# Kernel tuning notes

Hardware: AMD Instinct MI355X
Metric: run time of the kernel (lower is better)

Reference implementation:

```python
import jax, jax.numpy as jnp
import numpy as np

N = 50000          # residues
E = 1000000        # edges
H = 128            # hidden_channels
CUT = 11.5         # cutoff
NR = 6             # num_radial
NS = 3             # num_spherical
NPE = 16           # num_pos_emb

def swish(x):
    return x * jax.nn.sigmoid(x)

def rbf(d):
    # Bessel-style radial basis with smooth cosine cutoff, [E, NR]
    u = jnp.clip(d / CUT, 0.0, 1.0)
    n = jnp.arange(1, NR + 1, dtype=jnp.float32)
    fc = 0.5 * (jnp.cos(jnp.pi * u) + 1.0)
    return jnp.sqrt(2.0 / CUT) * jnp.sin(n * jnp.pi * u[:, None]) / (d[:, None] + 1e-6) * fc[:, None]

def angle_emb(d, ang):
    # d_angle_emb: radial x cos(l*angle) -> [E, NR*NS]
    r = rbf(d)
    l = jnp.arange(NS, dtype=jnp.float32)
    a = jnp.cos(ang[:, None] * l)
    return (r[:, :, None] * a[:, None, :]).reshape(d.shape[0], NR * NS)

def theta_phi_emb(d, theta, phi):
    # d_theta_phi_emb: radial x angular(theta) x angular(phi) -> [E, NR*NS*NS]
    r = rbf(d)
    l = jnp.arange(NS, dtype=jnp.float32)
    ct = jnp.cos(theta[:, None] * l)
    cp = jnp.cos(phi[:, None] * l)
    return jnp.einsum('en,el,em->enlm', r, ct, cp).reshape(d.shape[0], NR * NS * NS)


def setup_inputs():
    key = jax.random.key(0)
    ks = jax.random.split(key, 20)
    f32 = jnp.float32
    pos = jax.random.normal(ks[0], (N, 3), f32) * 8.0
    pos_n = pos + jax.random.normal(ks[1], (N, 3), f32) * 0.8
    pos_c = pos + jax.random.normal(ks[2], (N, 3), f32) * 0.8
    z = jax.random.randint(ks[3], (N,), 0, 26)
    bb_embs = jax.random.normal(ks[4], (N, 6), f32)
    side_chain_embs = jax.random.normal(ks[5], (N, 8), f32)
    esm_embs = jax.random.normal(ks[6], (N, 1280), f32)
    batch = jnp.zeros((N,), jnp.int32)
    edge_index = jax.random.randint(ks[7], (2, E), 0, N)
    def w(k, shape):
        return jax.random.normal(k, shape, f32) * (1.0 / np.sqrt(shape[0]))
    edge_in = NR * NS * NS + 3 * NR * NS + NPE  # 54 + 54 + 16 = 124
    params = dict(
        W_emb=w(ks[8], (26 + 6 + 8, H // 2)), b_emb=jnp.zeros((H // 2,), f32),
        W_esm=w(ks[9], (1280, H // 2)), b_esm=jnp.zeros((H // 2,), f32),
        W_edge=w(ks[10], (edge_in, H)),
        W_msg=w(ks[11], (H, H)),
        W_upd=w(ks[12], (H, H)),
        W_o0=w(ks[13], (H, H)), b_o0=jnp.zeros((H,), f32),
        W_o1=w(ks[14], (H, 32)), b_o1=jnp.zeros((32,), f32),
        W_of=w(ks[15], (32, 1)), b_of=jnp.zeros((1,), f32),
        W_n0=w(ks[16], (H, 32)), b_n0=jnp.zeros((32,), f32),
        W_nf=w(ks[17], (32, 2)), b_nf=jnp.zeros((2,), f32),
    )
    return dict(z=z, pos=pos, pos_n=pos_n, pos_c=pos_c, bb_embs=bb_embs,
                side_chain_embs=side_chain_embs, esm_embs=esm_embs,
                batch=batch, edge_index=edge_index, **params)


def reference(z, pos, pos_n, pos_c, bb_embs, side_chain_embs, esm_embs, batch,
              edge_index, W_emb, b_emb, W_esm, b_esm, W_edge, W_msg, W_upd,
              W_o0, b_o0, W_o1, b_o1, W_of, b_of, W_n0, b_n0, W_nf, b_nf):
    # --- node embedding fusion (level='allatom+esm') ---
    oh = jax.nn.one_hot(z, 26, dtype=jnp.float32)
    x_a = jnp.concatenate([oh, bb_embs, side_chain_embs], axis=1) @ W_emb + b_emb
    x_s = esm_embs @ W_esm + b_esm
    x = jnp.concatenate([x_a, x_s], axis=-1)  # [N, H]

    j, i = edge_index[0], edge_index[1]

    # --- sinusoidal positional embedding of sequence offsets ---
    dpe = (j - i).astype(jnp.float32)
    freq = jnp.exp(jnp.arange(0, NPE, 2, dtype=jnp.float32) * (-np.log(10000.0) / NPE))
    ang = dpe[:, None] * freq
    pe = jnp.concatenate([jnp.cos(ang), jnp.sin(ang)], axis=-1)  # [E, NPE]

    # --- distance / theta / phi (triplet gathers via sequence neighbors) ---
    v_ji = pos[j] - pos[i]
    dist = jnp.linalg.norm(pos[i] - pos[j], axis=1)
    refi0 = (i - 1) % N
    refi1 = (i + 1) % N
    v_r0 = pos[refi0] - pos[i]
    v_r1 = pos[refi1] - pos[i]
    a = jnp.sum(v_ji * v_r0, axis=-1)
    b = jnp.linalg.norm(jnp.cross(v_ji, v_r0), axis=-1)
    theta = jnp.arctan2(b, a)
    p1 = jnp.cross(v_r0, v_r1)
    p2 = jnp.cross(v_r0, v_ji)
    a = jnp.sum(p1 * p2, axis=-1)
    b = jnp.sum(jnp.cross(p1, p2) * v_r0, axis=-1) / (jnp.linalg.norm(v_r0, axis=-1) + 1e-7)
    phi = jnp.arctan2(b, a)
    feature0 = theta_phi_emb(dist, theta, phi)  # [E, 54]

    # --- backbone-frame Euler angles (allatom branch) ---
    o1x = pos_n[i] - pos[i]
    o1z = jnp.cross(o1x, jnp.cross(o1x, pos_c[i] - pos[i]))
    o1zl = jnp.linalg.norm(o1z, axis=1) + 1e-7
    o2x = pos_n[j] - pos[j]
    o2z = jnp.cross(o2x, jnp.cross(o2x, pos_c[j] - pos[j]))
    o2zl = jnp.linalg.norm(o2z, axis=1) + 1e-7
    nvec = jnp.cross(o1z, o2z)
    angle1 = jnp.arctan2(jnp.sum(jnp.cross(o1x, nvec) * o1z, -1) / o1zl, jnp.sum(o1x * nvec, -1))
    angle2 = jnp.arctan2(jnp.linalg.norm(nvec, axis=-1), jnp.sum(o1z * o2z, -1))
    angle3 = jnp.arctan2(jnp.sum(jnp.cross(nvec, o2x) * o2z, -1) / o2zl, jnp.sum(nvec * o2x, -1))
    feature1 = jnp.concatenate([angle_emb(dist, angle1), angle_emb(dist, angle2),
                                angle_emb(dist, angle3)], axis=1)  # [E, 54]

    # --- message passing (gather-compute-scatter stand-in for model_E) ---
    ef = swish(jnp.concatenate([feature0, feature1, pe], axis=-1) @ W_edge)  # [E, H]
    m = swish(x[j] @ W_msg) * ef
    agg = jax.ops.segment_sum(m, i, num_segments=N)
    xe = x + swish(agg @ W_upd)

    # --- output heads (dropout inactive at inference) ---
    xn = jax.nn.relu(x @ W_n0 + b_n0)
    node_out = xn @ W_nf + b_nf                   # [N, 2]
    h = jax.nn.relu(xe @ W_o0 + b_o0)
    h = jax.nn.relu(h @ W_o1 + b_o1)
    out = jax.nn.sigmoid(h @ W_of + b_of)         # [N, 1]
    return out, node_out
```

## Files before the change

kernel.cpp:

```cpp
#include <hip/hip_runtime.h>
#include <math.h>
#include <stdint.h>

#define NRES 50000
#define NEDGE 1000000
#define PI_F 3.14159265358979323846f
#define NSEG 196

typedef __attribute__((ext_vector_type(8))) short short8;
typedef __attribute__((ext_vector_type(4))) float floatx4;
typedef __attribute__((ext_vector_type(2))) short bf16x2;
typedef __attribute__((address_space(1))) bf16x2* gbf16x2p;

struct f3 { float x, y, z; };
__device__ __forceinline__ f3 ld3(const float* __restrict__ p, int i) {
  return {p[3*i+0], p[3*i+1], p[3*i+2]};
}
__device__ __forceinline__ f3 f3sub(f3 a, f3 b){ return {a.x-b.x, a.y-b.y, a.z-b.z}; }
__device__ __forceinline__ f3 f3cross(f3 a, f3 b){
  return {a.y*b.z - a.z*b.y, a.z*b.x - a.x*b.z, a.x*b.y - a.y*b.x};
}
__device__ __forceinline__ float f3dot(f3 a, f3 b){ return a.x*b.x + a.y*b.y + a.z*b.z; }
__device__ __forceinline__ float swish_fast(float v){
  return v * __builtin_amdgcn_rcpf(1.0f + __expf(-v));
}
__device__ __forceinline__ short f2bf(float f){
  unsigned u = __float_as_uint(f);
  unsigned r = (u + 0x7fffu + ((u >> 16) & 1u)) >> 16;
  return (short)r;
}
__device__ __forceinline__ float bf2f(short s){
  return __uint_as_float(((unsigned)(unsigned short)s) << 16);
}
__device__ __forceinline__ float cos_atan2(float y, float x){
  return x * __builtin_amdgcn_rsqf(fmaxf(x*x + y*y, 1e-30f));
}
__device__ __forceinline__ void atom_pk_bf16(short* addr, bf16x2 v){
  __builtin_amdgcn_global_atomic_fadd_v2bf16((gbf16x2p)(uintptr_t)addr, v);
}
__device__ __forceinline__ unsigned pkbf(float lo, float hi){
  unsigned r;
  asm("v_cvt_pk_bf16_f32 %0, %1, %2" : "=v"(r) : "v"(lo), "v"(hi));
  return r;
}

struct EdgeGeo {
  float rb[6];
  float ct, cp, ca1, ca2, ca3;
  float dpe;
};
__device__ __forceinline__ EdgeGeo edge_geo(
    int j, int i,
    const float* __restrict__ pos, const float* __restrict__ posn,
    const float* __restrict__ posc)
{
  EdgeGeo g;
  f3 pj = ld3(pos, j), pi = ld3(pos, i);
  f3 vji = f3sub(pj, pi);
  float nji2 = f3dot(vji, vji);
  float dist = sqrtf(nji2);
  int r0i = (i == 0) ? (NRES - 1) : (i - 1);
  int r1i = (i == NRES - 1) ? 0 : (i + 1);
  f3 vr0 = f3sub(ld3(pos, r0i), pi);
  f3 vr1 = f3sub(ld3(pos, r1i), pi);
  float nr02 = f3dot(vr0, vr0);

  g.ct = f3dot(vji, vr0) * __builtin_amdgcn_rsqf(fmaxf(nji2 * nr02, 1e-30f));
  f3 p1 = f3cross(vr0, vr1);
  f3 p2 = f3cross(vr0, vji);
  float pa = f3dot(p1, p2);
  float pb = f3dot(f3cross(p1, p2), vr0) / (sqrtf(nr02) + 1e-7f);
  g.cp = cos_atan2(pb, pa);

  f3 pni = ld3(posn, i), pci = ld3(posc, i);
  f3 o1x = f3sub(pni, pi);
  f3 o1z = f3cross(o1x, f3cross(o1x, f3sub(pci, pi)));
  float no1z2 = f3dot(o1z, o1z);
  float o1zl = sqrtf(no1z2) + 1e-7f;
  f3 pnj = ld3(posn, j), pcj = ld3(posc, j);
  f3 o2x = f3sub(pnj, pj);
  f3 o2z = f3cross(o2x, f3cross(o2x, f3sub(pcj, pj)));
  float no2z2 = f3dot(o2z, o2z);
  float o2zl = sqrtf(no2z2) + 1e-7f;
  f3 nv = f3cross(o1z, o2z);
  float y1 = f3dot(f3cross(o1x, nv), o1z) / o1zl;
  g.ca1 = cos_atan2(y1, f3dot(o1x, nv));
  g.ca2 = f3dot(o1z, o2z) * __builtin_amdgcn_rsqf(fmaxf(no1z2 * no2z2, 1e-30f));
  float y3 = f3dot(f3cross(nv, o2x), o2z) / o2zl;
  g.ca3 = cos_atan2(y3, f3dot(nv, o2x));

  float u = fminf(dist * (1.0f/11.5f), 1.0f);
  float spu, cpu;
  __sincosf(PI_F * u, &spu, &cpu);
  float fc = 0.5f * (cpu + 1.0f);
  float pref = 0.41702882811414954f * __builtin_amdgcn_rcpf(dist + 1e-6f) * fc;
  {
    float twoc = 2.0f * cpu;
    float s_nm1 = 0.0f, s_n = spu;
    #pragma unroll
    for (int nn = 0; nn < 6; ++nn) {
      g.rb[nn] = pref * s_n;
      float s_np1 = twoc * s_n - s_nm1;
      s_nm1 = s_n; s_n = s_np1;
    }
  }
  g.dpe = (float)(j - i);
  return g;
}

__device__ __forceinline__ float feat_val(const EdgeGeo& g, int f,
                                          const float* ctv, const float* cpv,
                                          const float* cav1, const float* cav2,
                                          const float* cav3)
{
  if (f < 54) {
    int nn = f / 9, l = (f % 9) / 3, m = f % 3;
    return g.rb[nn] * ctv[l] * cpv[m];
  } else {
    int ff = f - 54;
    int t = ff / 18, nn = (ff % 18) / 3, l = ff % 3;
    const float* cav = (t == 0) ? cav1 : (t == 1) ? cav2 : cav3;
    return g.rb[nn] * cav[l];
  }
}

__device__ __forceinline__ void edge_features_full(
    int e, int j, int i,
    const float* __restrict__ pos, const float* __restrict__ posn,
    const float* __restrict__ posc, short (*sF)[136])
{
  EdgeGeo g = edge_geo(j, i, pos, posn, posc);
  float ctv[3]  = {1.0f, g.ct,  2.0f*g.ct*g.ct  - 1.0f};
  float cpv[3]  = {1.0f, g.cp,  2.0f*g.cp*g.cp  - 1.0f};
  float cav1[3] = {1.0f, g.ca1, 2.0f*g.ca1*g.ca1 - 1.0f};
  float cav2[3] = {1.0f, g.ca2, 2.0f*g.ca2*g.ca2 - 1.0f};
  float cav3[3] = {1.0f, g.ca3, 2.0f*g.ca3*g.ca3 - 1.0f};
  #pragma unroll
  for (int f = 0; f < 108; f += 2) {
    float v0 = feat_val(g, f,     ctv, cpv, cav1, cav2, cav3);
    float v1 = feat_val(g, f + 1, ctv, cpv, cav1, cav2, cav3);
    *(unsigned*)&sF[e][f] = pkbf(v0, v1);
  }
  const float FRQ[8] = {1.0f, 0.31622776601683794f, 0.1f, 0.03162277660168379f,
                        0.01f, 0.003162277660168379f, 0.001f, 0.0003162277660168379f};
  float cb[8], sb[8];
  #pragma unroll
  for (int q = 0; q < 8; ++q) __sincosf(g.dpe * FRQ[q], &sb[q], &cb[q]);
  #pragma unroll
  for (int q = 0; q < 8; q += 2) {
    *(unsigned*)&sF[e][108 + q] = pkbf(cb[q], cb[q+1]);
    *(unsigned*)&sF[e][116 + q] = pkbf(sb[q], sb[q+1]);
  }
  *(unsigned*)&sF[e][124] = 0u;
  *(unsigned*)&sF[e][126] = 0u;
}

__device__ __forceinline__ void edge_features_q(
    int e, int j, int i, int q,
    const float* __restrict__ pos, const float* __restrict__ posn,
    const float* __restrict__ posc, short (*sF)[136])
{
  EdgeGeo g = edge_geo(j, i, pos, posn, posc);
  float ctv[3]  = {1.0f, g.ct,  2.0f*g.ct*g.ct  - 1.0f};
  float cpv[3]  = {1.0f, g.cp,  2.0f*g.cp*g.cp  - 1.0f};
  float cav1[3] = {1.0f, g.ca1, 2.0f*g.ca1*g.ca1 - 1.0f};
  float cav2[3] = {1.0f, g.ca2, 2.0f*g.ca2*g.ca2 - 1.0f};
  float cav3[3] = {1.0f, g.ca3, 2.0f*g.ca3*g.ca3 - 1.0f};

  if (q == 0) {
    #pragma unroll
    for (int f = 0; f < 28; f += 2)
      *(unsigned*)&sF[e][f] = pkbf(feat_val(g, f, ctv, cpv, cav1, cav2, cav3),
                                   feat_val(g, f+1, ctv, cpv, cav1, cav2, cav3));
  } else if (q == 1) {
    #pragma unroll
    for (int f = 28; f < 54; f += 2)
      *(unsigned*)&sF[e][f] = pkbf(feat_val(g, f, ctv, cpv, cav1, cav2, cav3),
                                   feat_val(g, f+1, ctv, cpv, cav1, cav2, cav3));
    const float FRQ[8] = {1.0f, 0.31622776601683794f, 0.1f, 0.03162277660168379f,
                          0.01f, 0.003162277660168379f, 0.001f, 0.0003162277660168379f};
    float cb[8], sb[8];
    #pragma unroll
    for (int p = 0; p < 8; ++p) __sincosf(g.dpe * FRQ[p], &sb[p], &cb[p]);
    #pragma unroll
    for (int p = 0; p < 8; p += 2) {
      *(unsigned*)&sF[e][108 + p] = pkbf(cb[p], cb[p+1]);
      *(unsigned*)&sF[e][116 + p] = pkbf(sb[p], sb[p+1]);
    }
    *(unsigned*)&sF[e][124] = 0u;
    *(unsigned*)&sF[e][126] = 0u;
  } else if (q == 2) {
    #pragma unroll
    for (int f = 54; f < 80; f += 2)
      *(unsigned*)&sF[e][f] = pkbf(feat_val(g, f, ctv, cpv, cav1, cav2, cav3),
                                   feat_val(g, f+1, ctv, cpv, cav1, cav2, cav3));
  } else {
    #pragma unroll
    for (int f = 80; f < 108; f += 2)
      *(unsigned*)&sF[e][f] = pkbf(feat_val(g, f, ctv, cpv, cav1, cav2, cav3),
                                   feat_val(g, f+1, ctv, cpv, cav1, cav2, cav3));
  }
}

__global__ __launch_bounds__(256) void k_wprep(
    const float* __restrict__ We, const float* __restrict__ Wm,
    const float* __restrict__ Ws, const float* __restrict__ Wu,
    const float* __restrict__ Wo0, const float* __restrict__ Wn0,
    const float* __restrict__ Wo1,
    short* __restrict__ Wef, short* __restrict__ Wmf, short* __restrict__ Wsf,
    short* __restrict__ Wuf, short* __restrict__ Wo0f,
    short* __restrict__ Wn0f, short* __restrict__ Wo1f)
{
  int gid = blockIdx.x * 256 + threadIdx.x;
  const float* src; short* dst; int NT, K, N, t;
  if      (gid < 16384)  { t = gid;          src = We;  dst = Wef;  NT = 8; K = 124;  N = 128; }
  else if (gid < 32768)  { t = gid - 16384;  src = Wm;  dst = Wmf;  NT = 8; K = 128;  N = 128; }
  else if (gid < 114688) { t = gid - 32768;  src = Ws;  dst = Wsf;  NT = 4; K = 1280; N = 64;  }
  else if (gid < 131072) { t = gid - 114688; src = Wu;  dst = Wuf;  NT = 8; K = 128;  N = 128; }
  else if (gid < 147456) { t = gid - 131072; src = Wo0; dst = Wo0f; NT = 8; K = 128;  N = 128; }
  else if (gid < 151552) { t = gid - 147456; src = Wn0; dst = Wn0f; NT = 2; K = 128;  N = 32;  }
  else if (gid < 155648) { t = gid - 151552; src = Wo1; dst = Wo1f; NT = 2; K = 128;  N = 32;  }
  else return;
  int j = t & 7, lane = (t >> 3) & 63;
  int rest = t >> 9;
  int nt = rest % NT, kt = rest / NT;
  int k = kt*32 + (lane >> 4)*8 + j, n = nt*16 + (lane & 15);
  dst[t] = f2bf((k < K) ? src[k*N + n] : 0.0f);
}

__global__ __launch_bounds__(256) void k_hist(
    const int* __restrict__ ei, int* __restrict__ bins)
{
  int e = blockIdx.x * 256 + threadIdx.x;
  if (e < NEDGE) atomicAdd(&bins[ei[NEDGE + e]], 1);
}

__global__ __launch_bounds__(256) void k_scan1(
    int* __restrict__ bins, int* __restrict__ bsum)
{
  __shared__ int s[256];
  const int t = threadIdx.x, b = blockIdx.x;
  const int idx = b * 256 + t;
  int v = (idx < NRES) ? bins[idx] : 0;
  s[t] = v;
  __syncthreads();
  #pragma unroll
  for (int d = 1; d < 256; d <<= 1) {
    int add = (t >= d) ? s[t - d] : 0;
    __syncthreads();
    if (t >= d) s[t] += add;
    __syncthreads();
  }
  if (idx < NRES) bins[idx] = s[t] - v;
  if (t == 255) bsum[b] = s[255];
}

__global__ __launch_bounds__(256) void k_scan2(int* __restrict__ bsum)
{
  __shared__ int s[256];
  const int t = threadIdx.x;
  int v = (t < NSEG) ? bsum[t] : 0;
  s[t] = v;
  __syncthreads();
  #pragma unroll
  for (int d = 1; d < 256; d <<= 1) {
    int add = (t >= d) ? s[t - d] : 0;
    __syncthreads();
    if (t >= d) s[t] += add;
    __syncthreads();
  }
  if (t < NSEG) bsum[t] = s[t] - v;
}

__global__ __launch_bounds__(256) void k_scatter(
    const int* __restrict__ ei, int* __restrict__ bins,
    const int* __restrict__ bsum, int2* __restrict__ sij)
{
  int e = blockIdx.x * 256 + threadIdx.x;
  if (e < NEDGE) {
    int j = ei[e], i = ei[NEDGE + e];
    int slot = atomicAdd(&bins[i], 1) + bsum[i >> 8];
    if (slot >= 0 && slot < NEDGE) sij[slot] = make_int2(j, i);
  }
}

__global__ __launch_bounds__(256) void k_xa(
    const int* __restrict__ z, const float* __restrict__ bb,
    const float* __restrict__ side, const float* __restrict__ W_emb,
    const float* __restrict__ b_emb, short* __restrict__ xb)
{
  int tid = threadIdx.x;
  int h = tid & 63;
  int n = blockIdx.x * 4 + (tid >> 6);
  if (n >= NRES) return;
  int zz = z[n];
  float acc = W_emb[zz * 64 + h] + b_emb[h];
  #pragma unroll
  for (int k = 0; k < 6; ++k) acc += bb[n*6 + k] * W_emb[(26 + k)*64 + h];
  #pragma unroll
  for (int k = 0; k < 8; ++k) acc += side[n*8 + k] * W_emb[(32 + k)*64 + h];
  xb[(size_t)n * 128 + h] = f2bf(acc);
}

__global__ __launch_bounds__(256) void k_esm(
    const float* __restrict__ esm, const short* __restrict__ Wsf,
    const float* __restrict__ b, short* __restrict__ xb)
{
  const int tid = threadIdx.x;
  const int lane = tid & 63, w = tid >> 6;
  const int quad = lane >> 4, colb = lane & 15;
  const int tile0 = blockIdx.x * 64 + w * 16;

  int arow = tile0 + colb;
  if (arow >= NRES) arow = NRES - 1;
  const float* ap = esm + (size_t)arow * 1280 + quad * 8;

  floatx4 acc[4];
  #pragma unroll
  for (int nt = 0; nt < 4; ++nt) acc[nt] = (floatx4){0.f, 0.f, 0.f, 0.f};

  for (int kt = 0; kt < 40; ++kt) {
    float4 v0 = *(const float4*)(ap + kt*32);
    float4 v1 = *(const float4*)(ap + kt*32 + 4);
    short8 a;
    a[0] = f2bf(v0.x); a[1] = f2bf(v0.y); a[2] = f2bf(v0.z); a[3] = f2bf(v0.w);
    a[4] = f2bf(v1.x); a[5] = f2bf(v1.y); a[6] = f2bf(v1.z); a[7] = f2bf(v1.w);
    #pragma unroll
    for (int nt = 0; nt < 4; ++nt) {
      short8 bf = *(const short8*)&Wsf[(size_t)((kt*4 + nt)*64 + lane)*8];
      acc[nt] = __builtin_amdgcn_mfma_f32_16x16x32_bf16(a, bf, acc[nt], 0, 0, 0);
    }
  }
  #pragma unroll
  for (int nt = 0; nt < 4; ++nt) {
    int ch = nt*16 + colb;
    float bias = b[ch];
    #pragma unroll
    for (int r = 0; r < 4; ++r) {
      int n = tile0 + quad*4 + r;
      if (n < NRES) xb[(size_t)n * 128 + 64 + ch] = f2bf(acc[nt][r] + bias);
    }
  }
}

__global__ __launch_bounds__(512) void k_node(
    const float* __restrict__ esm, const short* __restrict__ Wsf,
    const float* __restrict__ b_esm,
    const int* __restrict__ z, const float* __restrict__ bb,
    const float* __restrict__ side, const float* __restrict__ W_emb,
    const float* __restrict__ b_emb,
    const short* __restrict__ Wmf,
    short* __restrict__ xb, short* __restrict__ xmb)
{
  __shared__ __align__(16) short sE[2][64][72];
  __shared__ __align__(16) short sX[64][136];

  const int tid = threadIdx.x;
  const int lane = tid & 63, w = tid >> 6;
  const int quad = lane >> 4, colb = lane & 15;
  const int n0 = blockIdx.x * 64;

  const int lrow = tid >> 3;
  const int p0 = tid & 7, p1 = p0 + 8;
  int grow = n0 + lrow; if (grow >= NRES) grow = NRES - 1;
  const float* rbase = esm + (size_t)grow * 1280;

  const int rt = w & 3;
  const int ct0 = (w >> 2) * 2, ct1 = ct0 + 1;

  floatx4 acc0 = (floatx4){0.f,0.f,0.f,0.f};
  floatx4 acc1 = (floatx4){0.f,0.f,0.f,0.f};

  {
    float4 va = *(const float4*)(rbase + p0*4);
    float4 vb = *(const float4*)(rbase + p1*4);
    *(unsigned*)&sE[0][lrow][p0*4]     = pkbf(va.x, va.y);
    *(unsigned*)&sE[0][lrow][p0*4 + 2] = pkbf(va.z, va.w);
    *(unsigned*)&sE[0][lrow][p1*4]     = pkbf(vb.x, vb.y);
    *(unsigned*)&sE[0][lrow][p1*4 + 2] = pkbf(vb.z, vb.w);
  }
  __syncthreads();

  for (int s = 0; s < 20; ++s) {
    float4 va = {0.f,0.f,0.f,0.f}, vb = {0.f,0.f,0.f,0.f};
    if (s < 19) {
      va = *(const float4*)(rbase + (s+1)*64 + p0*4);
      vb = *(const float4*)(rbase + (s+1)*64 + p1*4);
    }
    const int buf = s & 1;
    #pragma unroll
    for (int kk = 0; kk < 2; ++kk) {
      short8 af = *(const short8*)&sE[buf][rt*16 + colb][kk*32 + quad*8];
      const int kc = s*2 + kk;
      short8 bf0 = *(const short8*)&Wsf[(size_t)((kc*4 + ct0)*64 + lane)*8];
      short8 bf1 = *(const short8*)&Wsf[(size_t)((kc*4 + ct1)*64 + lane)*8];
      acc0 = __builtin_amdgcn_mfma_f32_16x16x32_bf16(af, bf0, acc0, 0, 0, 0);
      acc1 = __builtin_amdgcn_mfma_f32_16x16x32_bf16(af, bf1, acc1, 0, 0, 0);
    }
    __syncthreads();
    if (s < 19) {
      const int nb = (s + 1) & 1;
      *(unsigned*)&sE[nb][lrow][p0*4]     = pkbf(va.x, va.y);
      *(unsigned*)&sE[nb][lrow][p0*4 + 2] = pkbf(va.z, va.w);
      *(unsigned*)&sE[nb][lrow][p1*4]     = pkbf(vb.x, vb.y);
      *(unsigned*)&sE[nb][lrow][p1*4 + 2] = pkbf(vb.z, vb.w);
      __syncthreads();
    }
  }

  {
    float bias0 = b_esm[ct0*16 + colb];
    float bias1 = b_esm[ct1*16 + colb];
    #pragma unroll
    for (int r = 0; r < 4; ++r) {
      int row = rt*16 + quad*4 + r;
      sX[row][64 + ct0*16 + colb] = f2bf(acc0[r] + bias0);
      sX[row][64 + ct1*16 + colb] = f2bf(acc1[r] + bias1);
    }
  }
  {
    int r2 = tid >> 3;
    int n2 = n0 + r2; if (n2 >= NRES) n2 = NRES - 1;
    int c0 = (tid & 7) * 8;
    int zz = z[n2];
    float bbv[6], sdv[8];
    #pragma unroll
    for (int k = 0; k < 6; ++k) bbv[k] = bb[n2*6 + k];
    #pragma unroll
    for (int k = 0; k < 8; ++k) sdv[k] = side[n2*8 + k];
    #pragma unroll
    for (int c = 0; c < 8; c += 2) {
      float u0, u1;
      #pragma unroll
      for (int h = 0; h < 2; ++h) {
        int col = c0 + c + h;
        float a2 = W_emb[zz*64 + col] + b_emb[col];
        #pragma unroll
        for (int k = 0; k < 6; ++k) a2 += bbv[k] * W_emb[(26 + k)*64 + col];
        #pragma unroll
        for (int k = 0; k < 8; ++k) a2 += sdv[k] * W_emb[(32 + k)*64 + col];
        if (h) u1 = a2; else u0 = a2;
      }
      *(unsigned*)&sX[r2][c0 + c] = pkbf(u0, u1);
    }
  }
  __syncthreads();

  #pragma unroll
  for (int it = 0; it < 2; ++it) {
    int idx = it * 512 + tid;
    int row = idx >> 4, c8 = idx & 15;
    int n = n0 + row;
    if (n < NRES) *(short8*)&xb[(size_t)n * 128 + c8*8] = *(const short8*)&sX[row][c8*8];
  }

  floatx4 accM[4];
  #pragma unroll
  for (int mt = 0; mt < 4; ++mt) accM[mt] = (floatx4){0.f,0.f,0.f,0.f};
  #pragma unroll
  for (int kt = 0; kt < 4; ++kt) {
    short8 b0 = *(const short8*)&Wmf[(size_t)((kt*8 + w)*64 + lane)*8];
    #pragma unroll
    for (int mt = 0; mt < 4; ++mt) {
      short8 a = *(const short8*)&sX[mt*16 + colb][kt*32 + quad*8];
      accM[mt] = __builtin_amdgcn_mfma_f32_16x16x32_bf16(a, b0, accM[mt], 0, 0, 0);
    }
  }
  __syncthreads();

  #pragma unroll
  for (int mt = 0; mt < 4; ++mt)
    #pragma unroll
    for (int r = 0; r < 4; ++r)
      sX[mt*16 + quad*4 + r][w*16 + colb] = f2bf(swish_fast(accM[mt][r]));
  __syncthreads();
  #pragma unroll
  for (int it = 0; it < 2; ++it) {
    int idx = it * 512 + tid;
    int row = idx >> 4, c8 = idx & 15;
    int n = n0 + row;
    if (n < NRES) *(short8*)&xmb[(size_t)n * 128 + c8*8] = *(const short8*)&sX[row][c8*8];
  }
}

__global__ __launch_bounds__(256, 4) void k_edge_s(
    const int2* __restrict__ sij,
    const float* __restrict__ pos,
    const float* __restrict__ posn, const float* __restrict__ posc,
    const short* __restrict__ xmb, const short* __restrict__ Wef,
    short* __restrict__ aggb)
{
  __shared__ int sJ[64];
  __shared__ int sI[64];
  __shared__ __align__(16) short sF[64][136];
  __shared__ __align__(16) short sXJ[64][136];

  const int tid = threadIdx.x;
  const int orig = blockIdx.x;
  const int xcd = orig & 7, sub = orig >> 3;
  const int wg = (xcd == 0 ? 0 : 1954 + (xcd - 1) * 1953) + sub;
  const int e0 = wg * 64;

  if (tid < 64) {
    int2 ji = sij[e0 + tid];
    int jj = ji.x, ii = ji.y;
    sJ[tid] = (jj < 0) ? 0 : ((jj >= NRES) ? NRES - 1 : jj);
    sI[tid] = (ii < 0) ? 0 : ((ii >= NRES) ? NRES - 1 : ii);
  }
  __syncthreads();

  {
    const int e = tid & 63, q = tid >> 6;
    edge_features_q(e, sJ[e], sI[e], q, pos, posn, posc, sF);
  }
  #pragma unroll
  for (int it = 0; it < 4; ++it) {
    int idx = it * 256 + tid;
    int row = idx >> 4;
    int c8 = idx & 15;
    *(short8*)&sXJ[row][c8*8] = *(const short8*)&xmb[(size_t)sJ[row] * 128 + c8*8];
  }
  __syncthreads();

  const int lane = tid & 63, w = tid >> 6;
  const int quad = lane >> 4, colb = lane & 15;
  const int nb = w * 2;

  short8 bE[4][2];
  #pragma unroll
  for (int kt = 0; kt < 4; ++kt)
    #pragma unroll
    for (int nt = 0; nt < 2; ++nt)
      bE[kt][nt] = *(const short8*)&Wef[(size_t)((kt*8 + nb + nt)*64 + lane)*8];

  floatx4 accE[4][2];
  #pragma unroll
  for (int mt = 0; mt < 4; ++mt) {
    accE[mt][0] = (floatx4){0.f, 0.f, 0.f, 0.f};
    accE[mt][1] = (floatx4){0.f, 0.f, 0.f, 0.f};
  }

  #pragma unroll
  for (int kt = 0; kt < 4; ++kt) {
    #pragma unroll
    for (int mt = 0; mt < 4; ++mt) {
      short8 af = *(const short8*)&sF[mt*16 + colb][kt*32 + quad*8];
      #pragma unroll
      for (int nt = 0; nt < 2; ++nt)
        accE[mt][nt] = __builtin_amdgcn_mfma_f32_16x16x32_bf16(af, bE[kt][nt], accE[mt][nt], 0, 0, 0);
    }
  }
  __syncthreads();

  short (*sM)[136] = sF;
  #pragma unroll
  for (int mt = 0; mt < 4; ++mt)
    #pragma unroll
    for (int nt = 0; nt < 2; ++nt) {
      int ch = w*32 + nt*16 + colb;
      #pragma unroll
      for (int r = 0; r < 4; ++r) {
        int e = mt*16 + quad*4 + r;
        float mv = bf2f(sXJ[e][ch]) * swish_fast(accE[mt][nt][r]);
        sM[e][ch] = f2bf(mv);
      }
    }
  __syncthreads();

  {
    const int p = tid & 63;
    const int g = tid >> 6;
    float ax = 0.f, ay = 0.f;
    int cur = sI[g * 16];
    #pragma unroll
    for (int rr = 0; rr < 16; ++rr) {
      int row = g * 16 + rr;
      int ii = sI[row];
      if (ii != cur) {
        bf16x2 v; v[0] = f2bf(ax); v[1] = f2bf(ay);
        atom_pk_bf16(&aggb[(size_t)cur * 128 + p*2], v);
        ax = 0.f; ay = 0.f; cur = ii;
      }
      bf16x2 mv = *(const bf16x2*)&sM[row][p*2];
      ax += bf2f(mv[0]); ay += bf2f(mv[1]);
    }
    bf16x2 v; v[0] = f2bf(ax); v[1] = f2bf(ay);
    atom_pk_bf16(&aggb[(size_t)cur * 128 + p*2], v);
  }
}

__global__ __launch_bounds__(256, 4) void k_edge_b(
    const int* __restrict__ ei, const float* __restrict__ pos,
    const float* __restrict__ posn, const float* __restrict__ posc,
    const short* __restrict__ xb, const short* __restrict__ Wef,
    const short* __restrict__ Wmf, short* __restrict__ aggb)
{
  __shared__ int sJ[64];
  __shared__ int sI[64];
  __shared__ __align__(16) short sF[64][136];
  __shared__ __align__(16) short sXJ[64][136];

  const int tid = threadIdx.x;
  const int e0 = blockIdx.x * 64;

  if (tid < 64) { sJ[tid] = ei[e0 + tid]; sI[tid] = ei[NEDGE + e0 + tid]; }
  __syncthreads();

  if (tid < 64) {
    edge_features_full(tid, sJ[tid], sI[tid], pos, posn, posc, sF);
  } else {
    const int t2 = tid - 64;
    for (int it = 0; it < 6; ++it) {
      int idx = it * 192 + t2;
      if (idx < 1024) {
        int row = idx >> 4;
        int c8 = idx & 15;
        *(short8*)&sXJ[row][c8*8] = *(const short8*)&xb[(size_t)sJ[row] * 128 + c8*8];
      }
    }
  }
  __syncthreads();

  const int lane = tid & 63, w = tid >> 6;
  const int quad = lane >> 4, colb = lane & 15;
  const int nb = w * 2;

  short8 bE[4][2], bM[4][2];
  #pragma unroll
  for (int kt = 0; kt < 4; ++kt)
    #pragma unroll
    for (int nt = 0; nt < 2; ++nt) {
      bE[kt][nt] = *(const short8*)&Wef[(size_t)((kt*8 + nb + nt)*64 + lane)*8];
      bM[kt][nt] = *(const short8*)&Wmf[(size_t)((kt*8 + nb + nt)*64 + lane)*8];
    }

  floatx4 accE[4][2], accM[4][2];
  #pragma unroll
  for (int mt = 0; mt < 4; ++mt)
    #pragma unroll
    for (int nt = 0; nt < 2; ++nt) {
      accE[mt][nt] = (floatx4){0.f, 0.f, 0.f, 0.f};
      accM[mt][nt] = (floatx4){0.f, 0.f, 0.f, 0.f};
    }

  #pragma unroll
  for (int kt = 0; kt < 4; ++kt) {
    #pragma unroll
    for (int mt = 0; mt < 4; ++mt) {
      short8 af = *(const short8*)&sF [mt*16 + colb][kt*32 + quad*8];
      short8 ax = *(const short8*)&sXJ[mt*16 + colb][kt*32 + quad*8];
      #pragma unroll
      for (int nt = 0; nt < 2; ++nt) {
        accE[mt][nt] = __builtin_amdgcn_mfma_f32_16x16x32_bf16(af, bE[kt][nt], accE[mt][nt], 0, 0, 0);
        accM[mt][nt] = __builtin_amdgcn_mfma_f32_16x16x32_bf16(ax, bM[kt][nt], accM[mt][nt], 0, 0, 0);
      }
    }
  }
  __syncthreads();

  short (*sM)[136] = sXJ;
  #pragma unroll
  for (int mt = 0; mt < 4; ++mt)
    #pragma unroll
    for (int nt = 0; nt < 2; ++nt) {
      int ch = w*32 + nt*16 + colb;
      #pragma unroll
      for (int r = 0; r < 4; ++r) {
        int e = mt*16 + quad*4 + r;
        sM[e][ch] = f2bf(swish_fast(accM[mt][nt][r]) * swish_fast(accE[mt][nt][r]));
      }
    }
  __syncthreads();

  #pragma unroll
  for (int it = 0; it < 16; ++it) {
    int flat = it * 256 + tid;
    int row = flat >> 6, p = flat & 63;
    bf16x2 v = *(const bf16x2*)&sM[row][p*2];
    atom_pk_bf16(&aggb[(size_t)sI[row] * 128 + p*2], v);
  }
}

__global__ __launch_bounds__(256) void k_upd(
    const short* __restrict__ xb, const short* __restrict__ aggb,
    const short* __restrict__ Wuf, const short* __restrict__ Wo0f,
    const short* __restrict__ Wn0f, const short* __restrict__ Wo1f,
    const float* __restrict__ bn0, const float* __restrict__ Wnf,
    const float* __restrict__ bnf, const float* __restrict__ bo0,
    const float* __restrict__ bo1, const float* __restrict__ Wof,
    const float* __restrict__ bof, float* __restrict__ out0,
    float* __restrict__ out1)
{
  __shared__ __align__(16) short sA[64][136];
  __shared__ __align__(16) short sX[64][136];
  __shared__ float sS[64][33];

  const int tid = threadIdx.x;
  const int lane = tid & 63, w = tid >> 6;
  const int quad = lane >> 4, colb = lane & 15;
  const int n0 = blockIdx.x * 64;

  #pragma unroll
  for (int it = 0; it < 4; ++it) {
    int idx = it * 256 + tid;
    int row = idx >> 4, c8 = idx & 15;
    int n = n0 + row;
    short8 va = (short8)(short)0, vx = (short8)(short)0;
    if (n < NRES) {
      va = *(const short8*)&aggb[(size_t)n * 128 + c8*8];
      vx = *(const short8*)&xb  [(size_t)n * 128 + c8*8];
    }
    *(short8*)&sA[row][c8*8] = va;
    *(short8*)&sX[row][c8*8] = vx;
  }
  __syncthreads();

  {
    floatx4 accN[2];
    accN[0] = (floatx4){0.f,0.f,0.f,0.f}; accN[1] = (floatx4){0.f,0.f,0.f,0.f};
    #pragma unroll
    for (int kt = 0; kt < 4; ++kt) {
      short8 a = *(const short8*)&sX[w*16 + colb][kt*32 + quad*8];
      #pragma unroll
      for (int nt = 0; nt < 2; ++nt) {
        short8 bf = *(const short8*)&Wn0f[(size_t)((kt*2 + nt)*64 + lane)*8];
        accN[nt] = __builtin_amdgcn_mfma_f32_16x16x32_bf16(a, bf, accN[nt], 0, 0, 0);
      }
    }
    #pragma unroll
    for (int nt = 0; nt < 2; ++nt) {
      int col = nt*16 + colb;
      float bias = bn0[col];
      #pragma unroll
      for (int r = 0; r < 4; ++r)
        sS[w*16 + quad*4 + r][col] = fmaxf(accN[nt][r] + bias, 0.0f);
    }
  }
  __syncthreads();
  if (tid < 128) {
    int row = tid >> 1, oc = tid & 1;
    int n = n0 + row;
    if (n < NRES) {
      float a2 = bnf[oc];
      #pragma unroll
      for (int k = 0; k < 32; ++k) a2 += sS[row][k] * Wnf[k*2 + oc];
      out1[(size_t)n * 2 + oc] = a2;
    }
  }

  floatx4 acc1[4][2];
  #pragma unroll
  for (int mt = 0; mt < 4; ++mt) {
    acc1[mt][0] = (floatx4){0.f,0.f,0.f,0.f};
    acc1[mt][1] = (floatx4){0.f,0.f,0.f,0.f};
  }
  #pragma unroll
  for (int kt = 0; kt < 4; ++kt) {
    short8 b0 = *(const short8*)&Wuf[(size_t)((kt*8 + w*2 + 0)*64 + lane)*8];
    short8 b1 = *(const short8*)&Wuf[(size_t)((kt*8 + w*2 + 1)*64 + lane)*8];
    #pragma unroll
    for (int mt = 0; mt < 4; ++mt) {
      short8 a = *(const short8*)&sA[mt*16 + colb][kt*32 + quad*8];
      acc1[mt][0] = __builtin_amdgcn_mfma_f32_16x16x32_bf16(a, b0, acc1[mt][0], 0, 0, 0);
      acc1[mt][1] = __builtin_amdgcn_mfma_f32_16x16x32_bf16(a, b1, acc1[mt][1], 0, 0, 0);
    }
  }
  __syncthreads();
  #pragma unroll
  for (int mt = 0; mt < 4; ++mt)
    #pragma unroll
    for (int nt = 0; nt < 2; ++nt)
      #pragma unroll
      for (int r = 0; r < 4; ++r) {
        int row = mt*16 + quad*4 + r, col = w*32 + nt*16 + colb;
        float xv = bf2f(sX[row][col]);
        sA[row][col] = f2bf(xv + swish_fast(acc1[mt][nt][r]));
      }
  __syncthreads();

  floatx4 acc2[4][2];
  #pragma unroll
  for (int mt = 0; mt < 4; ++mt) {
    acc2[mt][0] = (floatx4){0.f,0.f,0.f,0.f};
    acc2[mt][1] = (floatx4){0.f,0.f,0.f,0.f};
  }
  #pragma unroll
  for (int kt = 0; kt < 4; ++kt) {
    short8 b0 = *(const short8*)&Wo0f[(size_t)((kt*8 + w*2 + 0)*64 + lane)*8];
    short8 b1 = *(const short8*)&Wo0f[(size_t)((kt*8 + w*2 + 1)*64 + lane)*8];
    #pragma unroll
    for (int mt = 0; mt < 4; ++mt) {
      short8 a = *(const short8*)&sA[mt*16 + colb][kt*32 + quad*8];
      acc2[mt][0] = __builtin_amdgcn_mfma_f32_16x16x32_bf16(a, b0, acc2[mt][0], 0, 0, 0);
      acc2[mt][1] = __builtin_amdgcn_mfma_f32_16x16x32_bf16(a, b1, acc2[mt][1], 0, 0, 0);
    }
  }
  __syncthreads();
  #pragma unroll
  for (int mt = 0; mt < 4; ++mt)
    #pragma unroll
    for (int nt = 0; nt < 2; ++nt) {
      int col = w*32 + nt*16 + colb;
      float bias = bo0[col];
      #pragma unroll
      for (int r = 0; r < 4; ++r) {
        int row = mt*16 + quad*4 + r;
        sX[row][col] = f2bf(fmaxf(acc2[mt][nt][r] + bias, 0.0f));
      }
    }
  __syncthreads();

  {
    floatx4 accH[2];
    accH[0] = (floatx4){0.f,0.f,0.f,0.f}; accH[1] = (floatx4){0.f,0.f,0.f,0.f};
    #pragma unroll
    for (int kt = 0; kt < 4; ++kt) {
      short8 a = *(const short8*)&sX[w*16 + colb][kt*32 + quad*8];
      #pragma unroll
      for (int nt = 0; nt < 2; ++nt) {
        short8 bf = *(const short8*)&Wo1f[(size_t)((kt*2 + nt)*64 + lane)*8];
        accH[nt] = __builtin_amdgcn_mfma_f32_16x16x32_bf16(a, bf, accH[nt], 0, 0, 0);
      }
    }
    __syncthreads();
    #pragma unroll
    for (int nt = 0; nt < 2; ++nt) {
      int col = nt*16 + colb;
      float bias = bo1[col];
      #pragma unroll
      for (int r = 0; r < 4; ++r)
        sS[w*16 + quad*4 + r][col] = fmaxf(accH[nt][r] + bias, 0.0f);
    }
  }
  __syncthreads();

  if (tid < 64) {
    int n = n0 + tid;
    if (n < NRES) {
      float a2 = bof[0];
      #pragma unroll
      for (int k = 0; k < 32; ++k) a2 += sS[tid][k] * Wof[k];
      out0[n] = 1.0f / (1.0f + expf(-a2));
    }
  }
}

extern "C" void kernel_launch(void* const* d_in, const int* in_sizes, int n_in,
                              void* d_out, int out_size, void* d_ws, size_t ws_size,
                              hipStream_t stream) {
  (void)in_sizes; (void)n_in; (void)out_size;
  const int*   z     = (const int*)  d_in[0];
  const float* pos   = (const float*)d_in[1];
  const float* posn  = (const float*)d_in[2];
  const float* posc  = (const float*)d_in[3];
  const float* bb    = (const float*)d_in[4];
  const float* side  = (const float*)d_in[5];
  const float* esm   = (const float*)d_in[6];
  const int*   ei    = (const int*)  d_in[8];
  const float* W_emb = (const float*)d_in[9];
  const float* b_emb = (const float*)d_in[10];
  const float* W_esm = (const float*)d_in[11];
  const float* b_esm = (const float*)d_in[12];
  const float* W_edge= (const float*)d_in[13];
  const float* W_msg = (const float*)d_in[14];
  const float* W_upd = (const float*)d_in[15];
  const float* W_o0  = (const float*)d_in[16];
  const float* b_o0  = (const float*)d_in[17];
  const float* W_o1  = (const float*)d_in[18];
  const float* b_o1  = (const float*)d_in[19];
  const float* W_of  = (const float*)d_in[20];
  const float* b_of  = (const float*)d_in[21];
  const float* W_n0  = (const float*)d_in[22];
  const float* b_n0  = (const float*)d_in[23];
  const float* W_nf  = (const float*)d_in[24];
  const float* b_nf  = (const float*)d_in[25];

  float* out0 = (float*)d_out;
  float* out1 = out0 + NRES;
  char* ws = (char*)d_ws;

  const bool full = (ws_size >= (size_t)46912096);

  if (full) {
    short* xb   = (short*)ws;
    short* aggb = (short*)(ws + 12800000);
    short* xmb  = (short*)(ws + 25600000);
    short* Wef  = (short*)(ws + 38400000);
    short* Wmf  = (short*)(ws + 38432768);
    short* Wsf  = (short*)(ws + 38465536);
    short* Wuf  = (short*)(ws + 38629376);
    short* Wo0f = (short*)(ws + 38662144);
    short* Wn0f = (short*)(ws + 38694912);
    short* Wo1f = (short*)(ws + 38703104);
    int*   bins = (int*)  (ws + 38711296);
    int*   bsum = (int*)  (ws + 38911296);
    int2*  sij  = (int2*) (ws + 38912096);

    hipMemsetAsync(aggb, 0, (size_t)NRES * 128 * sizeof(short), stream);
    hipMemsetAsync(bins, 0, (size_t)NRES * sizeof(int), stream);

    k_wprep  <<<608, 256, 0, stream>>>(W_edge, W_msg, W_esm, W_upd, W_o0, W_n0, W_o1,
                                       Wef, Wmf, Wsf, Wuf, Wo0f, Wn0f, Wo1f);
    k_hist   <<<3907, 256, 0, stream>>>(ei, bins);
    k_scan1  <<<NSEG, 256, 0, stream>>>(bins, bsum);
    k_scan2  <<<1,    256, 0, stream>>>(bsum);
    k_scatter<<<3907, 256, 0, stream>>>(ei, bins, bsum, sij);
    k_node   <<<782,  512, 0, stream>>>(esm, Wsf, b_esm, z, bb, side, W_emb, b_emb,
                                        Wmf, xb, xmb);
    k_edge_s <<<15625, 256, 0, stream>>>(sij, pos, posn, posc, xmb, Wef, aggb);
    k_upd    <<<782,   256, 0, stream>>>(xb, aggb, Wuf, Wo0f, Wn0f, Wo1f,
                                         b_n0, W_nf, b_nf, b_o0, b_o1, W_of, b_of,
                                         out0, out1);
  } else {
    short* xb   = (short*)ws;
    short* aggb = (short*)(ws + 12800000);
    short* Wef  = (short*)(ws + 25600000);
    short* Wmf  = (short*)(ws + 25632768);
    short* Wsf  = (short*)(ws + 25665536);
    short* Wuf  = (short*)(ws + 25829376);
    short* Wo0f = (short*)(ws + 25862144);
    short* Wn0f = (short*)(ws + 25894912);
    short* Wo1f = (short*)(ws + 25903104);

    hipMemsetAsync(aggb, 0, (size_t)NRES * 128 * sizeof(short), stream);

    k_wprep <<<608, 256, 0, stream>>>(W_edge, W_msg, W_esm, W_upd, W_o0, W_n0, W_o1,
                                      Wef, Wmf, Wsf, Wuf, Wo0f, Wn0f, Wo1f);
    k_xa    <<<12500, 256, 0, stream>>>(z, bb, side, W_emb, b_emb, xb);
    k_esm   <<<782,   256, 0, stream>>>(esm, Wsf, b_esm, xb);
    k_edge_b<<<15625, 256, 0, stream>>>(ei, pos, posn, posc, xb, Wef, Wmf, aggb);
    k_upd   <<<782,   256, 0, stream>>>(xb, aggb, Wuf, Wo0f, Wn0f, Wo1f,
                                        b_n0, W_nf, b_nf, b_o0, b_o1, W_of, b_of,
                                        out0, out1);
  }
}
```

Before: 675.5 us.

## Fuse weight prep and counting sort into one cooperative kernel with grid syncs

Replaces five separate launches (weight repack, histogram, two scan passes, scatter) with a single cooperative kernel of 1024 blocks that uses grid-wide syncs between phases. This is meant to remove kernel launch gaps and tail effects between the small sort kernels. It keeps the original multi-kernel path as a fallback if the cooperative launch fails. The cost is grid.sync overhead and grid-stride loops running on fewer threads. The edge_features functions are only reordered.

```diff
diff --git a/kernel.cpp b/kernel.cpp
--- a/kernel.cpp
+++ b/kernel.cpp
@@ -1,6 +1,9 @@
 #include <hip/hip_runtime.h>
+#include <hip/hip_cooperative_groups.h>
 #include <math.h>
 #include <stdint.h>
+
+namespace cg = cooperative_groups;
 
 #define NRES 50000
 #define NEDGE 1000000
@@ -124,8 +127,8 @@
   }
 }
 
-__device__ __forceinline__ void edge_features_full(
-    int e, int j, int i,
+__device__ __forceinline__ void edge_features_q(
+    int e, int j, int i, int q,
     const float* __restrict__ pos, const float* __restrict__ posn,
     const float* __restrict__ posc, short (*sF)[136])
 {
@@ -135,28 +138,44 @@
   float cav1[3] = {1.0f, g.ca1, 2.0f*g.ca1*g.ca1 - 1.0f};
   float cav2[3] = {1.0f, g.ca2, 2.0f*g.ca2*g.ca2 - 1.0f};
   float cav3[3] = {1.0f, g.ca3, 2.0f*g.ca3*g.ca3 - 1.0f};
-  #pragma unroll
-  for (int f = 0; f < 108; f += 2) {
-    float v0 = feat_val(g, f,     ctv, cpv, cav1, cav2, cav3);
-    float v1 = feat_val(g, f + 1, ctv, cpv, cav1, cav2, cav3);
-    *(unsigned*)&sF[e][f] = pkbf(v0, v1);
-  }
-  const float FRQ[8] = {1.0f, 0.31622776601683794f, 0.1f, 0.03162277660168379f,
-                        0.01f, 0.003162277660168379f, 0.001f, 0.0003162277660168379f};
-  float cb[8], sb[8];
-  #pragma unroll
-  for (int q = 0; q < 8; ++q) __sincosf(g.dpe * FRQ[q], &sb[q], &cb[q]);
-  #pragma unroll
-  for (int q = 0; q < 8; q += 2) {
-    *(unsigned*)&sF[e][108 + q] = pkbf(cb[q], cb[q+1]);
-    *(unsigned*)&sF[e][116 + q] = pkbf(sb[q], sb[q+1]);
-  }
-  *(unsigned*)&sF[e][124] = 0u;
-  *(unsigned*)&sF[e][126] = 0u;
-}
-
-__device__ __forceinline__ void edge_features_q(
-    int e, int j, int i, int q,
+
+  if (q == 0) {
+    #pragma unroll
+    for (int f = 0; f < 28; f += 2)
+      *(unsigned*)&sF[e][f] = pkbf(feat_val(g, f, ctv, cpv, cav1, cav2, cav3),
+                                   feat_val(g, f+1, ctv, cpv, cav1, cav2, cav3));
+  } else if (q == 1) {
+    #pragma unroll
+    for (int f = 28; f < 54; f += 2)
+      *(unsigned*)&sF[e][f] = pkbf(feat_val(g, f, ctv, cpv, cav1, cav2, cav3),
+                                   feat_val(g, f+1, ctv, cpv, cav1, cav2, cav3));
+    const float FRQ[8] = {1.0f, 0.31622776601683794f, 0.1f, 0.03162277660168379f,
+                          0.01f, 0.003162277660168379f, 0.001f, 0.0003162277660168379f};
+    float cb[8], sb[8];
+    #pragma unroll
+    for (int p = 0; p < 8; ++p) __sincosf(g.dpe * FRQ[p], &sb[p], &cb[p]);
+    #pragma unroll
+    for (int p = 0; p < 8; p += 2) {
+      *(unsigned*)&sF[e][108 + p] = pkbf(cb[p], cb[p+1]);
+      *(unsigned*)&sF[e][116 + p] = pkbf(sb[p], sb[p+1]);
+    }
+    *(unsigned*)&sF[e][124] = 0u;
+    *(unsigned*)&sF[e][126] = 0u;
+  } else if (q == 2) {
+    #pragma unroll
+    for (int f = 54; f < 80; f += 2)
+      *(unsigned*)&sF[e][f] = pkbf(feat_val(g, f, ctv, cpv, cav1, cav2, cav3),
+                                   feat_val(g, f+1, ctv, cpv, cav1, cav2, cav3));
+  } else {
+    #pragma unroll
+    for (int f = 80; f < 108; f += 2)
+      *(unsigned*)&sF[e][f] = pkbf(feat_val(g, f, ctv, cpv, cav1, cav2, cav3),
+                                   feat_val(g, f+1, ctv, cpv, cav1, cav2, cav3));
+  }
+}
+
+__device__ __forceinline__ void edge_features_full(
+    int e, int j, int i,
     const float* __restrict__ pos, const float* __restrict__ posn,
     const float* __restrict__ posc, short (*sF)[136])
 {
@@ -166,39 +185,111 @@
   float cav1[3] = {1.0f, g.ca1, 2.0f*g.ca1*g.ca1 - 1.0f};
   float cav2[3] = {1.0f, g.ca2, 2.0f*g.ca2*g.ca2 - 1.0f};
   float cav3[3] = {1.0f, g.ca3, 2.0f*g.ca3*g.ca3 - 1.0f};
-
-  if (q == 0) {
-    #pragma unroll
-    for (int f = 0; f < 28; f += 2)
-      *(unsigned*)&sF[e][f] = pkbf(feat_val(g, f, ctv, cpv, cav1, cav2, cav3),
-                                   feat_val(g, f+1, ctv, cpv, cav1, cav2, cav3));
-  } else if (q == 1) {
-    #pragma unroll
-    for (int f = 28; f < 54; f += 2)
-      *(unsigned*)&sF[e][f] = pkbf(feat_val(g, f, ctv, cpv, cav1, cav2, cav3),
-                                   feat_val(g, f+1, ctv, cpv, cav1, cav2, cav3));
-    const float FRQ[8] = {1.0f, 0.31622776601683794f, 0.1f, 0.03162277660168379f,
-                          0.01f, 0.003162277660168379f, 0.001f, 0.0003162277660168379f};
-    float cb[8], sb[8];
-    #pragma unroll
-    for (int p = 0; p < 8; ++p) __sincosf(g.dpe * FRQ[p], &sb[p], &cb[p]);
-    #pragma unroll
-    for (int p = 0; p < 8; p += 2) {
-      *(unsigned*)&sF[e][108 + p] = pkbf(cb[p], cb[p+1]);
-      *(unsigned*)&sF[e][116 + p] = pkbf(sb[p], sb[p+1]);
-    }
-    *(unsigned*)&sF[e][124] = 0u;
-    *(unsigned*)&sF[e][126] = 0u;
-  } else if (q == 2) {
-    #pragma unroll
-    for (int f = 54; f < 80; f += 2)
-      *(unsigned*)&sF[e][f] = pkbf(feat_val(g, f, ctv, cpv, cav1, cav2, cav3),
-                                   feat_val(g, f+1, ctv, cpv, cav1, cav2, cav3));
-  } else {
-    #pragma unroll
-    for (int f = 80; f < 108; f += 2)
-      *(unsigned*)&sF[e][f] = pkbf(feat_val(g, f, ctv, cpv, cav1, cav2, cav3),
-                                   feat_val(g, f+1, ctv, cpv, cav1, cav2, cav3));
+  #pragma unroll
+  for (int f = 0; f < 108; f += 2) {
+    float v0 = feat_val(g, f,     ctv, cpv, cav1, cav2, cav3);
+    float v1 = feat_val(g, f + 1, ctv, cpv, cav1, cav2, cav3);
+    *(unsigned*)&sF[e][f] = pkbf(v0, v1);
+  }
+  const float FRQ[8] = {1.0f, 0.31622776601683794f, 0.1f, 0.03162277660168379f,
+                        0.01f, 0.003162277660168379f, 0.001f, 0.0003162277660168379f};
+  float cb[8], sb[8];
+  #pragma unroll
+  for (int q = 0; q < 8; ++q) __sincosf(g.dpe * FRQ[q], &sb[q], &cb[q]);
+  #pragma unroll
+  for (int q = 0; q < 8; q += 2) {
+    *(unsigned*)&sF[e][108 + q] = pkbf(cb[q], cb[q+1]);
+    *(unsigned*)&sF[e][116 + q] = pkbf(sb[q], sb[q+1]);
+  }
+  *(unsigned*)&sF[e][124] = 0u;
+  *(unsigned*)&sF[e][126] = 0u;
+}
+
+__device__ __forceinline__ void wprep_item(
+    int gid,
+    const float* __restrict__ We, const float* __restrict__ Wm,
+    const float* __restrict__ Ws, const float* __restrict__ Wu,
+    const float* __restrict__ Wo0, const float* __restrict__ Wn0,
+    const float* __restrict__ Wo1,
+    short* __restrict__ Wef, short* __restrict__ Wmf, short* __restrict__ Wsf,
+    short* __restrict__ Wuf, short* __restrict__ Wo0f,
+    short* __restrict__ Wn0f, short* __restrict__ Wo1f)
+{
+  const float* src; short* dst; int NT, K, N, t;
+  if      (gid < 16384)  { t = gid;          src = We;  dst = Wef;  NT = 8; K = 124;  N = 128; }
+  else if (gid < 32768)  { t = gid - 16384;  src = Wm;  dst = Wmf;  NT = 8; K = 128;  N = 128; }
+  else if (gid < 114688) { t = gid - 32768;  src = Ws;  dst = Wsf;  NT = 4; K = 1280; N = 64;  }
+  else if (gid < 131072) { t = gid - 114688; src = Wu;  dst = Wuf;  NT = 8; K = 128;  N = 128; }
+  else if (gid < 147456) { t = gid - 131072; src = Wo0; dst = Wo0f; NT = 8; K = 128;  N = 128; }
+  else if (gid < 151552) { t = gid - 147456; src = Wn0; dst = Wn0f; NT = 2; K = 128;  N = 32;  }
+  else                   { t = gid - 151552; src = Wo1; dst = Wo1f; NT = 2; K = 128;  N = 32;  }
+  int j = t & 7, lane = (t >> 3) & 63;
+  int rest = t >> 9;
+  int nt = rest % NT, kt = rest / NT;
+  int k = kt*32 + (lane >> 4)*8 + j, n = nt*16 + (lane & 15);
+  dst[t] = f2bf((k < K) ? src[k*N + n] : 0.0f);
+}
+
+__global__ __launch_bounds__(256) void k_sort_coop(
+    const float* __restrict__ We, const float* __restrict__ Wm,
+    const float* __restrict__ Ws, const float* __restrict__ Wu,
+    const float* __restrict__ Wo0, const float* __restrict__ Wn0,
+    const float* __restrict__ Wo1,
+    short* __restrict__ Wef, short* __restrict__ Wmf, short* __restrict__ Wsf,
+    short* __restrict__ Wuf, short* __restrict__ Wo0f,
+    short* __restrict__ Wn0f, short* __restrict__ Wo1f,
+    const int* __restrict__ ei, int* __restrict__ bins,
+    int* __restrict__ bsum, int2* __restrict__ sij)
+{
+  cg::grid_group grid = cg::this_grid();
+  __shared__ int s[256];
+  const int tid = threadIdx.x;
+  const int gidx = blockIdx.x * 256 + tid;
+  const int gstride = gridDim.x * 256;
+
+  for (int it = gidx; it < 155648; it += gstride)
+    wprep_item(it, We, Wm, Ws, Wu, Wo0, Wn0, Wo1,
+               Wef, Wmf, Wsf, Wuf, Wo0f, Wn0f, Wo1f);
+  for (int e = gidx; e < NEDGE; e += gstride)
+    atomicAdd(&bins[ei[NEDGE + e]], 1);
+  grid.sync();
+
+  if (blockIdx.x < NSEG) {
+    const int idx = blockIdx.x * 256 + tid;
+    int v = (idx < NRES) ? bins[idx] : 0;
+    s[tid] = v;
+    __syncthreads();
+    #pragma unroll
+    for (int d = 1; d < 256; d <<= 1) {
+      int add = (tid >= d) ? s[tid - d] : 0;
+      __syncthreads();
+      if (tid >= d) s[tid] += add;
+      __syncthreads();
+    }
+    if (idx < NRES) bins[idx] = s[tid] - v;
+    if (tid == 255) bsum[blockIdx.x] = s[255];
+  }
+  grid.sync();
+
+  if (blockIdx.x == 0) {
+    int v = (tid < NSEG) ? bsum[tid] : 0;
+    s[tid] = v;
+    __syncthreads();
+    #pragma unroll
+    for (int d = 1; d < 256; d <<= 1) {
+      int add = (tid >= d) ? s[tid - d] : 0;
+      __syncthreads();
+      if (tid >= d) s[tid] += add;
+      __syncthreads();
+    }
+    if (tid < NSEG) bsum[tid] = s[tid] - v;
+  }
+  grid.sync();
+
+  for (int e = gidx; e < NEDGE; e += gstride) {
+    int j = ei[e], i = ei[NEDGE + e];
+    int slot = atomicAdd(&bins[i], 1) + bsum[i >> 8];
+    if (slot >= 0 && slot < NEDGE) sij[slot] = make_int2(j, i);
   }
 }
 
@@ -212,20 +303,9 @@
     short* __restrict__ Wn0f, short* __restrict__ Wo1f)
 {
   int gid = blockIdx.x * 256 + threadIdx.x;
-  const float* src; short* dst; int NT, K, N, t;
-  if      (gid < 16384)  { t = gid;          src = We;  dst = Wef;  NT = 8; K = 124;  N = 128; }
-  else if (gid < 32768)  { t = gid - 16384;  src = Wm;  dst = Wmf;  NT = 8; K = 128;  N = 128; }
-  else if (gid < 114688) { t = gid - 32768;  src = Ws;  dst = Wsf;  NT = 4; K = 1280; N = 64;  }
-  else if (gid < 131072) { t = gid - 114688; src = Wu;  dst = Wuf;  NT = 8; K = 128;  N = 128; }
-  else if (gid < 147456) { t = gid - 131072; src = Wo0; dst = Wo0f; NT = 8; K = 128;  N = 128; }
-  else if (gid < 151552) { t = gid - 147456; src = Wn0; dst = Wn0f; NT = 2; K = 128;  N = 32;  }
-  else if (gid < 155648) { t = gid - 151552; src = Wo1; dst = Wo1f; NT = 2; K = 128;  N = 32;  }
-  else return;
-  int j = t & 7, lane = (t >> 3) & 63;
-  int rest = t >> 9;
-  int nt = rest % NT, kt = rest / NT;
-  int k = kt*32 + (lane >> 4)*8 + j, n = nt*16 + (lane & 15);
-  dst[t] = f2bf((k < K) ? src[k*N + n] : 0.0f);
+  if (gid < 155648)
+    wprep_item(gid, We, Wm, Ws, Wu, Wo0, Wn0, Wo1,
+               Wef, Wmf, Wsf, Wuf, Wo0f, Wn0f, Wo1f);
 }
 
 __global__ __launch_bounds__(256) void k_hist(
@@ -899,12 +979,26 @@
     hipMemsetAsync(aggb, 0, (size_t)NRES * 128 * sizeof(short), stream);
     hipMemsetAsync(bins, 0, (size_t)NRES * sizeof(int), stream);
 
-    k_wprep  <<<608, 256, 0, stream>>>(W_edge, W_msg, W_esm, W_upd, W_o0, W_n0, W_o1,
-                                       Wef, Wmf, Wsf, Wuf, Wo0f, Wn0f, Wo1f);
-    k_hist   <<<3907, 256, 0, stream>>>(ei, bins);
-    k_scan1  <<<NSEG, 256, 0, stream>>>(bins, bsum);
-    k_scan2  <<<1,    256, 0, stream>>>(bsum);
-    k_scatter<<<3907, 256, 0, stream>>>(ei, bins, bsum, sij);
+    void* ca[] = {
+      (void*)&W_edge, (void*)&W_msg, (void*)&W_esm, (void*)&W_upd,
+      (void*)&W_o0, (void*)&W_n0, (void*)&W_o1,
+      (void*)&Wef, (void*)&Wmf, (void*)&Wsf, (void*)&Wuf,
+      (void*)&Wo0f, (void*)&Wn0f, (void*)&Wo1f,
+      (void*)&ei, (void*)&bins, (void*)&bsum, (void*)&sij
+    };
+    hipError_t cerr = hipLaunchCooperativeKernel(
+        (const void*)k_sort_coop, dim3(1024), dim3(256), ca, 0, stream);
+    if (cerr != hipSuccess) {
+      (void)hipGetLastError();
+      k_wprep  <<<608, 256, 0, stream>>>(W_edge, W_msg, W_esm, W_upd, W_o0,
+                                         W_n0, W_o1, Wef, Wmf, Wsf, Wuf,
+                                         Wo0f, Wn0f, Wo1f);
+      k_hist   <<<3907, 256, 0, stream>>>(ei, bins);
+      k_scan1  <<<NSEG, 256, 0, stream>>>(bins, bsum);
+      k_scan2  <<<1,    256, 0, stream>>>(bsum);
+      k_scatter<<<3907, 256, 0, stream>>>(ei, bins, bsum, sij);
+    }
+
     k_node   <<<782,  512, 0, stream>>>(esm, Wsf, b_esm, z, bb, side, W_emb, b_emb,
                                         Wmf, xb, xmb);
     k_edge_s <<<15625, 256, 0, stream>>>(sij, pos, posn, posc, xmb, Wef, aggb);
```

Measured after the change: 1.034 ms. 1.53x slower.
